# Optimization experiments

Hardware: AMD Instinct MI355X
Metric: run time of the kernel (lower is better)

## Reference

```python
import math
import jax, jax.numpy as jnp
import numpy as np

H, D_MODEL, D_K, D_V, SEQ, BATCH = 12, 768, 64, 64, 2048, 4


def setup_inputs() -> dict:
    key = jax.random.key(0)
    k1, k2, k3, k4, k5 = jax.random.split(key, 5)
    s = math.sqrt(0.02)
    return {
        "residual": jax.random.normal(k1, (BATCH, SEQ, D_MODEL), dtype=jnp.float32),
        "W_Q": jax.random.normal(k2, (H, D_MODEL, D_K), dtype=jnp.float32) * s,
        "W_K": jax.random.normal(k3, (H, D_MODEL, D_K), dtype=jnp.float32) * s,
        "W_V": jax.random.normal(k4, (H, D_MODEL, D_V), dtype=jnp.float32) * s,
        "W_O": jax.random.normal(k5, (H * D_V, D_MODEL), dtype=jnp.float32) * s,
    }


def reference(residual, W_Q, W_K, W_V, W_O):
    B, S, _ = residual.shape
    # Projections: h=head, m=d_model, k=d_k/d_v
    Q = jnp.einsum("hmk,bsm->hbsk", W_Q, residual)
    K = jnp.einsum("hmk,bsm->hbsk", W_K, residual)
    V = jnp.einsum("hmv,bsm->hbsv", W_V, residual)
    # Scores [h, b, s_q, s_k] + additive causal mask, scaled BEFORE softmax
    QK = jnp.einsum("hbqk,hbsk->hbqs", Q, K)
    causal = jnp.triu(jnp.ones((S, S), dtype=bool), k=1)
    mask = jnp.where(causal, -jnp.inf, 0.0).astype(QK.dtype)  # broadcasts over h,b
    soft = jax.nn.softmax((QK + mask) / math.sqrt(D_K), axis=-1)
    attn = jnp.einsum("hbqs,hbsv->hbqv", soft, V)
    # [h,b,q,v] -> [b,q,h*v]
    multi_head = jnp.transpose(attn, (1, 2, 0, 3)).reshape(B, S, -1)
    return jnp.einsum("nd,bqn->bqd", W_O, multi_head)
```

## Files before the change

kernel.cpp:

```cpp
#include <hip/hip_runtime.h>

typedef _Float16 f16;
typedef __fp16 h16x2 __attribute__((ext_vector_type(2)));
typedef _Float16 f16x8 __attribute__((ext_vector_type(8)));
typedef float f32x4 __attribute__((ext_vector_type(4)));

#define H_ 12
#define B_ 4
#define S_ 2048
#define DM 768
#define DK 64
#define HBSD ((size_t)H_ * B_ * S_ * DK)

__device__ __forceinline__ f16 f2h(float f) { return (f16)f; }

__device__ __forceinline__ void gl_lds16(const f16* g, f16* l) {
  __builtin_amdgcn_global_load_lds(
      (const __attribute__((address_space(1))) void*)g,
      (__attribute__((address_space(3))) void*)l, 16, 0, 0);
}


__global__ __launch_bounds__(256) void cast_x_kernel(const float* __restrict__ x,
                                                     f16* __restrict__ xb, int n4) {
  int i = blockIdx.x * 256 + threadIdx.x;
  if (i < n4) {
    float4 v = ((const float4*)x)[i];
    union { f16 h[4]; uint2 u; } pk;
    pk.h[0] = f2h(v.x); pk.h[1] = f2h(v.y); pk.h[2] = f2h(v.z); pk.h[3] = f2h(v.w);
    ((uint2*)xb)[i] = pk.u;
  }
}

__global__ __launch_bounds__(256) void tcast_qkv_kernel(const float* __restrict__ WQ,
                                                        const float* __restrict__ WK,
                                                        const float* __restrict__ WV,
                                                        f16* __restrict__ Wt) {
  __shared__ float L[64][65];
  const int m0 = blockIdx.x * 64, which = blockIdx.y, h = blockIdx.z;
  const float* in = (which == 0 ? WQ : which == 1 ? WK : WV) + (size_t)h * DM * DK;
  const int t = threadIdx.x;
  const int lr = t >> 2, lc = (t & 3) * 16;
  const float* ip = in + (size_t)(m0 + lr) * DK + lc;
#pragma unroll
  for (int i = 0; i < 4; i++) {
    float4 v = *(const float4*)(ip + i * 4);
    L[lr][lc + i * 4 + 0] = v.x;
    L[lr][lc + i * 4 + 1] = v.y;
    L[lr][lc + i * 4 + 2] = v.z;
    L[lr][lc + i * 4 + 3] = v.w;
  }
  __syncthreads();
  const int oc = t >> 2, om = (t & 3) * 16;
  union { f16 hh[16]; uint4 u[2]; } pk;
#pragma unroll
  for (int jx = 0; jx < 16; jx++) pk.hh[jx] = f2h(L[om + jx][oc]);
  f16* op = Wt + ((size_t)which * DM + h * DK + oc) * DM + m0 + om;
  *(uint4*)op = pk.u[0];
  *(uint4*)(op + 8) = pk.u[1];
}

__global__ __launch_bounds__(256) void tcast_wo_kernel(const float* __restrict__ WO,
                                                       f16* __restrict__ Wt) {
  __shared__ float L[64][65];
  const int n0 = blockIdx.x * 64, d0 = blockIdx.y * 64;
  const int t = threadIdx.x;
  const int lr = t >> 2, lc = (t & 3) * 16;
  const float* ip = WO + (size_t)(n0 + lr) * DM + d0 + lc;
#pragma unroll
  for (int i = 0; i < 4; i++) {
    float4 v = *(const float4*)(ip + i * 4);
    L[lr][lc + i * 4 + 0] = v.x;
    L[lr][lc + i * 4 + 1] = v.y;
    L[lr][lc + i * 4 + 2] = v.z;
    L[lr][lc + i * 4 + 3] = v.w;
  }
  __syncthreads();
  const int oc = t >> 2, om = (t & 3) * 16;
  union { f16 hh[16]; uint4 u[2]; } pk;
#pragma unroll
  for (int jx = 0; jx < 16; jx++) pk.hh[jx] = f2h(L[om + jx][oc]);
  f16* op = Wt + (size_t)(d0 + oc) * DM + n0 + om;
  *(uint4*)op = pk.u[0];
  *(uint4*)(op + 8) = pk.u[1];
}

template <int MODE>
__global__ __launch_bounds__(256) void gemm_bt_kernel(const f16* __restrict__ A,
                                                      const f16* __restrict__ Bt,
                                                      float* __restrict__ Cf,
                                                      f16* __restrict__ Cq,
                                                      f16* __restrict__ Vt, int N) {
  constexpr int K = 768;
  __shared__ __align__(16) f16 As[2 * 128 * 32];
  __shared__ __align__(16) f16 Bs[2 * 128 * 32];
  const int t = threadIdx.x;
  const int m0 = blockIdx.y * 128, n0 = blockIdx.x * 128;
  const int lane = t & 63, wave = t >> 6;
  const int l15 = lane & 15, quad = lane >> 4;
  const int qsw = quad ^ ((l15 >> 1) & 3);
  const int m_off = (wave & 1) * 64, n_off = (wave >> 1) * 64;
  const int r0 = t >> 2, ko = ((t & 3) ^ ((t >> 3) & 3)) * 8;
  const f16* Ag0 = A + (size_t)(m0 + r0) * K + ko;
  const f16* Ag1 = A + (size_t)(m0 + r0 + 64) * K + ko;
  const f16* Bg0 = Bt + (size_t)(n0 + r0) * K + ko;
  const f16* Bg1 = Bt + (size_t)(n0 + r0 + 64) * K + ko;

  f32x4 acc[4][4];
  const f32x4 z4 = {0.f, 0.f, 0.f, 0.f};
  for (int i = 0; i < 4; i++)
    for (int j = 0; j < 4; j++) acc[i][j] = z4;

  for (int kt = 0; kt < K; kt += 64) {
    __syncthreads();
#pragma unroll
    for (int s = 0; s < 2; s++) {
      gl_lds16(Ag0 + kt + s * 32, &As[s * 4096 + t * 8]);
      gl_lds16(Ag1 + kt + s * 32, &As[s * 4096 + 2048 + t * 8]);
      gl_lds16(Bg0 + kt + s * 32, &Bs[s * 4096 + t * 8]);
      gl_lds16(Bg1 + kt + s * 32, &Bs[s * 4096 + 2048 + t * 8]);
    }
    __syncthreads();
#pragma unroll
    for (int s = 0; s < 2; s++) {
      f16x8 af[4], bfr[4];
#pragma unroll
      for (int i = 0; i < 4; i++)
        af[i] = *(const f16x8*)&As[s * 4096 + (m_off + i * 16 + l15) * 32 + qsw * 8];
#pragma unroll
      for (int i = 0; i < 4; i++)
        bfr[i] = *(const f16x8*)&Bs[s * 4096 + (n_off + i * 16 + l15) * 32 + qsw * 8];
#pragma unroll
      for (int mi = 0; mi < 4; mi++)
#pragma unroll
        for (int ni = 0; ni < 4; ni++)
          acc[mi][ni] = __builtin_amdgcn_mfma_f32_16x16x32_f16(af[mi], bfr[ni],
                                                               acc[mi][ni], 0, 0, 0);
    }
  }

  if (MODE == 0) {
#pragma unroll
    for (int mi = 0; mi < 4; mi++) {
      int row = m0 + m_off + mi * 16 + quad * 4;
#pragma unroll
      for (int ni = 0; ni < 4; ni++) {
        int col = n0 + n_off + ni * 16 + l15;
#pragma unroll
        for (int r = 0; r < 4; r++) Cf[(size_t)(row + r) * N + col] = acc[mi][ni][r];
      }
    }
  } else {
#pragma unroll
    for (int mi = 0; mi < 4; mi++) {
      int srow = m0 + m_off + mi * 16 + quad * 4;
      int bb = srow >> 11, ss = srow & 2047;
#pragma unroll
      for (int ni = 0; ni < 4; ni++) {
        int n = n0 + n_off + ni * 16 + l15;
        int which = n / DM;
        int rr = n - which * DM;
        int h = rr >> 6, kk = rr & 63;
        if (which < 2) {
#pragma unroll
          for (int r = 0; r < 4; r++) {
            size_t dst = (size_t)which * HBSD +
                         ((size_t)((h * B_ + bb) * S_) + ss + r) * DK + kk;
            Cq[dst] = f2h(acc[mi][ni][r]);
          }
        } else {
          union { f16 hh[4]; uint2 u; } pk;
#pragma unroll
          for (int r = 0; r < 4; r++) pk.hh[r] = f2h(acc[mi][ni][r]);
          *(uint2*)&Vt[((size_t)(h * B_ + bb) * DK + kk) * S_ + ss] = pk.u;
        }
      }
    }
  }
}

__global__ __launch_bounds__(256, 3) void flash_kernel(const f16* __restrict__ Qg,
                                                       const f16* __restrict__ Kg,
                                                       const f16* __restrict__ Vtg,
                                                       f16* __restrict__ MH) {
  __shared__ __align__(16) f16 Ksh[2 * 64 * 32];
  __shared__ __align__(16) f16 Vsh[2 * 64 * 32];
  __shared__ __align__(16) f16 Ps[4][16 * 72];

  const int t = threadIdx.x, lane = t & 63, w = t >> 6;
  const int l15 = lane & 15, quad = lane >> 4;
  const int qsw = quad ^ ((l15 >> 1) & 3);
  const int bid = blockIdx.x;
  const int xcd = bid & 7, gi = bid >> 3;
  const int hbi = gi % 6, pr = gi / 6;
  const int hb = xcd * 6 + hbi;
  const int qbA = pr, qbB = 31 - pr;
  const int h = hb >> 2, b = hb & 3;
  const size_t base = (size_t)hb * S_ * DK;
  const f16* Qp = Qg + base;
  const f16* Kp = Kg + base;
  const f16* Vp = Vtg + base;
  const float c2 = 0.18033688011f;

  f16x8 aqA[2], aqB[2];
  {
    const f16* qa = Qp + (size_t)(qbA * 64 + w * 16 + l15) * DK + quad * 8;
    aqA[0] = *(const f16x8*)(qa);
    aqA[1] = *(const f16x8*)(qa + 32);
    const f16* qb_ = Qp + (size_t)(qbB * 64 + w * 16 + l15) * DK + quad * 8;
    aqB[0] = *(const f16x8*)(qb_);
    aqB[1] = *(const f16x8*)(qb_ + 32);
  }
  const int qlaneA = qbA * 64 + w * 16 + l15;
  const int qlaneB = qbB * 64 + w * 16 + l15;

  const int srow = t >> 2, scol = ((t & 3) ^ ((t >> 3) & 3)) * 8;
  const f16* Kst = Kp + (size_t)srow * DK + scol;
  const f16* Vst = Vp + (size_t)srow * S_ + scol;

  float mA = -1e30f, lA = 0.f, mB = -1e30f, lB = 0.f;
  f32x4 oA[4], oB[4];
  const f32x4 z4 = {0.f, 0.f, 0.f, 0.f};
#pragma unroll
  for (int ni = 0; ni < 4; ni++) { oA[ni] = z4; oB[ni] = z4; }

  auto do_job = [&](const f16x8* aq, float& m_s, float& l_s, f32x4* oacc,
                    int qlane, int kv0, bool diag) {
    f32x4 sa[4];
#pragma unroll
    for (int mi = 0; mi < 4; mi++) {
      f16x8 k0 = *(const f16x8*)&Ksh[(mi * 16 + l15) * 32 + qsw * 8];
      sa[mi] = __builtin_amdgcn_mfma_f32_16x16x32_f16(k0, aq[0], z4, 0, 0, 0);
    }
#pragma unroll
    for (int mi = 0; mi < 4; mi++) {
      f16x8 k1 = *(const f16x8*)&Ksh[2048 + (mi * 16 + l15) * 32 + qsw * 8];
      sa[mi] = __builtin_amdgcn_mfma_f32_16x16x32_f16(k1, aq[1], sa[mi], 0, 0, 0);
    }

    if (diag) {
#pragma unroll
      for (int mi = 0; mi < 4; mi++)
#pragma unroll
        for (int r = 0; r < 4; r++)
          if (kv0 + mi * 16 + quad * 4 + r > qlane) sa[mi][r] = -1e30f;
    }

    float mx = fmaxf(fmaxf(fmaxf(sa[0][0], sa[0][1]), fmaxf(sa[0][2], sa[0][3])),
                     fmaxf(fmaxf(sa[1][0], sa[1][1]), fmaxf(sa[1][2], sa[1][3])));
    float mx2 = fmaxf(fmaxf(fmaxf(sa[2][0], sa[2][1]), fmaxf(sa[2][2], sa[2][3])),
                      fmaxf(fmaxf(sa[3][0], sa[3][1]), fmaxf(sa[3][2], sa[3][3])));
    mx = fmaxf(mx, mx2);
    mx = fmaxf(mx, __shfl_xor(mx, 16));
    mx = fmaxf(mx, __shfl_xor(mx, 32));
    float pm = mx * c2;
    if (!__all(pm <= m_s + 8.f)) {
      float m2 = fmaxf(m_s, pm);
      float alpha = __builtin_exp2f(m_s - m2);
      l_s *= alpha;
#pragma unroll
      for (int ni = 0; ni < 4; ni++)
#pragma unroll
        for (int r = 0; r < 4; r++) oacc[ni][r] *= alpha;
      m_s = m2;
    }
    const float m2 = m_s;
    float rs = 0.f;
#pragma unroll
    for (int mi = 0; mi < 4; mi++)
#pragma unroll
      for (int r = 0; r < 4; r++) {
        float p = __builtin_exp2f(fmaf(sa[mi][r], c2, -m2));
        sa[mi][r] = p;
        rs += p;
      }
    rs += __shfl_xor(rs, 16);
    rs += __shfl_xor(rs, 32);
    l_s += rs;

#pragma unroll
    for (int mi = 0; mi < 4; mi++) {
      union { h16x2 h2[2]; uint2 u; } pk;
      pk.h2[0] = __builtin_amdgcn_cvt_pkrtz(sa[mi][0], sa[mi][1]);
      pk.h2[1] = __builtin_amdgcn_cvt_pkrtz(sa[mi][2], sa[mi][3]);
      *(uint2*)&Ps[w][l15 * 72 + mi * 16 + quad * 4] = pk.u;
    }

#pragma unroll
    for (int kc2 = 0; kc2 < 2; kc2++) {
      f16x8 ap = *(const f16x8*)&Ps[w][l15 * 72 + kc2 * 32 + quad * 8];
#pragma unroll
      for (int ni = 0; ni < 4; ni++) {
        f16x8 vf = *(const f16x8*)&Vsh[kc2 * 2048 + (ni * 16 + l15) * 32 + qsw * 8];
        oacc[ni] = __builtin_amdgcn_mfma_f32_16x16x32_f16(vf, ap, oacc[ni], 0, 0, 0);
      }
    }
  };

  for (int kt = 0; kt <= qbB; kt++) {
    const int kv0 = kt * 64;
    __syncthreads();
    gl_lds16(Kst + (size_t)kv0 * DK, &Ksh[t * 8]);
    gl_lds16(Kst + (size_t)kv0 * DK + 32, &Ksh[2048 + t * 8]);
    gl_lds16(Vst + kv0, &Vsh[t * 8]);
    gl_lds16(Vst + kv0 + 32, &Vsh[2048 + t * 8]);
    __syncthreads();

    do_job(aqB, mB, lB, oB, qlaneB, kv0, kt == qbB);
    if (kt <= qbA) do_job(aqA, mA, lA, oA, qlaneA, kv0, kt == qbA);
  }

  {
    float linv = 1.0f / lB;
    f16* dst = MH + ((size_t)b * S_ + qlaneB) * DM + h * DK + quad * 4;
#pragma unroll
    for (int ni = 0; ni < 4; ni++) {
      union { f16 hh[4]; uint2 u; } pk;
#pragma unroll
      for (int r = 0; r < 4; r++) pk.hh[r] = f2h(oB[ni][r] * linv);
      *(uint2*)(dst + ni * 16) = pk.u;
    }
  }
  {
    float linv = 1.0f / lA;
    f16* dst = MH + ((size_t)b * S_ + qlaneA) * DM + h * DK + quad * 4;
#pragma unroll
    for (int ni = 0; ni < 4; ni++) {
      union { f16 hh[4]; uint2 u; } pk;
#pragma unroll
      for (int r = 0; r < 4; r++) pk.hh[r] = f2h(oA[ni][r] * linv);
      *(uint2*)(dst + ni * 16) = pk.u;
    }
  }
}


extern "C" void kernel_launch(void* const* d_in, const int* in_sizes, int n_in,
                              void* d_out, int out_size, void* d_ws, size_t ws_size,
                              hipStream_t stream) {
  const float* residual = (const float*)d_in[0];
  const float* WQ = (const float*)d_in[1];
  const float* WK = (const float*)d_in[2];
  const float* WV = (const float*)d_in[3];
  const float* WO = (const float*)d_in[4];
  float* out = (float*)d_out;

  char* ws = (char*)d_ws;
  size_t off = 0;
  auto alloc = [&](size_t bytes) {
    void* p = ws + off;
    off += (bytes + 255) & ~(size_t)255;
    return p;
  };
  f16* xb = (f16*)alloc((size_t)B_ * S_ * DM * 2);
  f16* wqkv = (f16*)alloc((size_t)3 * DM * DM * 2);
  f16* wot = (f16*)alloc((size_t)DM * DM * 2);
  f16* qk = (f16*)alloc(2 * HBSD * 2);
  f16* vt = (f16*)alloc(HBSD * 2);
  f16* mh = (f16*)alloc((size_t)B_ * S_ * DM * 2);

  cast_x_kernel<<<(B_ * S_ * DM / 4 + 255) / 256, 256, 0, stream>>>(residual, xb,
                                                                    B_ * S_ * DM / 4);
  tcast_qkv_kernel<<<dim3(DM / 64, 3, H_), 256, 0, stream>>>(WQ, WK, WV, wqkv);
  tcast_wo_kernel<<<dim3(DM / 64, DM / 64), 256, 0, stream>>>(WO, wot);

  gemm_bt_kernel<1><<<dim3(3 * DM / 128, B_ * S_ / 128), 256, 0, stream>>>(
      xb, wqkv, nullptr, qk, vt, 3 * DM);

  flash_kernel<<<768, 256, 0, stream>>>(qk, qk + HBSD, vt, mh);

  gemm_bt_kernel<0><<<dim3(DM / 128, B_ * S_ / 128), 256, 0, stream>>>(
      mh, wot, out, nullptr, nullptr, DM);
}
```

Measured before the change: 217.3 us.

## Double-buffer K/V tiles in flash kernel with async prefetch and setprio

Splits the K and V shared-memory tiles into two buffers and issues the next tile's global-to-LDS loads before computing on the current one, waiting only on the older loads via a partial vmcnt. This aims to hide global load latency behind the MFMA work instead of stalling after each load. The MFMA sections are also wrapped in s_setprio, and the row-max is rewritten as a tree of three-input maxes. LDS use doubles for K/V, which may lower occupancy, and the hand-written waitcnt and barrier sequencing has to be exactly right to avoid races.

Result: slower. 228.0 us (+4.9%).

```diff
diff --git a/kernel.cpp b/kernel.cpp
--- a/kernel.cpp
+++ b/kernel.cpp
@@ -13,6 +13,9 @@
 #define HBSD ((size_t)H_ * B_ * S_ * DK)
 
 __device__ __forceinline__ f16 f2h(float f) { return (f16)f; }
+__device__ __forceinline__ float max3f(float a, float b, float c) {
+  return fmaxf(fmaxf(a, b), c);
+}
 
 __device__ __forceinline__ void gl_lds16(const f16* g, f16* l) {
   __builtin_amdgcn_global_load_lds(
@@ -183,8 +186,8 @@
                                                        const f16* __restrict__ Kg,
                                                        const f16* __restrict__ Vtg,
                                                        f16* __restrict__ MH) {
-  __shared__ __align__(16) f16 Ksh[2 * 64 * 32];
-  __shared__ __align__(16) f16 Vsh[2 * 64 * 32];
+  __shared__ __align__(16) f16 Ksh[2][4096];
+  __shared__ __align__(16) f16 Vsh[2][4096];
   __shared__ __align__(16) f16 Ps[4][16 * 72];
 
   const int t = threadIdx.x, lane = t & 63, w = t >> 6;
@@ -224,19 +227,28 @@
 #pragma unroll
   for (int ni = 0; ni < 4; ni++) { oA[ni] = z4; oB[ni] = z4; }
 
-  auto do_job = [&](const f16x8* aq, float& m_s, float& l_s, f32x4* oacc,
+  auto stage = [&](int buf, int kv0) {
+    gl_lds16(Kst + (size_t)kv0 * DK, &Ksh[buf][t * 8]);
+    gl_lds16(Kst + (size_t)kv0 * DK + 32, &Ksh[buf][2048 + t * 8]);
+    gl_lds16(Vst + kv0, &Vsh[buf][t * 8]);
+    gl_lds16(Vst + kv0 + 32, &Vsh[buf][2048 + t * 8]);
+  };
+
+  auto do_job = [&](int buf, const f16x8* aq, float& m_s, float& l_s, f32x4* oacc,
                     int qlane, int kv0, bool diag) {
     f32x4 sa[4];
-#pragma unroll
-    for (int mi = 0; mi < 4; mi++) {
-      f16x8 k0 = *(const f16x8*)&Ksh[(mi * 16 + l15) * 32 + qsw * 8];
+    __builtin_amdgcn_s_setprio(1);
+#pragma unroll
+    for (int mi = 0; mi < 4; mi++) {
+      f16x8 k0 = *(const f16x8*)&Ksh[buf][(mi * 16 + l15) * 32 + qsw * 8];
       sa[mi] = __builtin_amdgcn_mfma_f32_16x16x32_f16(k0, aq[0], z4, 0, 0, 0);
     }
 #pragma unroll
     for (int mi = 0; mi < 4; mi++) {
-      f16x8 k1 = *(const f16x8*)&Ksh[2048 + (mi * 16 + l15) * 32 + qsw * 8];
+      f16x8 k1 = *(const f16x8*)&Ksh[buf][2048 + (mi * 16 + l15) * 32 + qsw * 8];
       sa[mi] = __builtin_amdgcn_mfma_f32_16x16x32_f16(k1, aq[1], sa[mi], 0, 0, 0);
     }
+    __builtin_amdgcn_s_setprio(0);
 
     if (diag) {
 #pragma unroll
@@ -246,11 +258,12 @@
           if (kv0 + mi * 16 + quad * 4 + r > qlane) sa[mi][r] = -1e30f;
     }
 
-    float mx = fmaxf(fmaxf(fmaxf(sa[0][0], sa[0][1]), fmaxf(sa[0][2], sa[0][3])),
-                     fmaxf(fmaxf(sa[1][0], sa[1][1]), fmaxf(sa[1][2], sa[1][3])));
-    float mx2 = fmaxf(fmaxf(fmaxf(sa[2][0], sa[2][1]), fmaxf(sa[2][2], sa[2][3])),
-                      fmaxf(fmaxf(sa[3][0], sa[3][1]), fmaxf(sa[3][2], sa[3][3])));
-    mx = fmaxf(mx, mx2);
+    float g0 = max3f(sa[0][0], sa[0][1], sa[0][2]);
+    float g1 = max3f(sa[0][3], sa[1][0], sa[1][1]);
+    float g2 = max3f(sa[1][2], sa[1][3], sa[2][0]);
+    float g3 = max3f(sa[2][1], sa[2][2], sa[2][3]);
+    float g4 = max3f(sa[3][0], sa[3][1], sa[3][2]);
+    float mx = fmaxf(max3f(g0, g1, g2), max3f(g3, g4, sa[3][3]));
     mx = fmaxf(mx, __shfl_xor(mx, 16));
     mx = fmaxf(mx, __shfl_xor(mx, 32));
     float pm = mx * c2;
@@ -286,28 +299,35 @@
       *(uint2*)&Ps[w][l15 * 72 + mi * 16 + quad * 4] = pk.u;
     }
 
+    __builtin_amdgcn_s_setprio(1);
 #pragma unroll
     for (int kc2 = 0; kc2 < 2; kc2++) {
       f16x8 ap = *(const f16x8*)&Ps[w][l15 * 72 + kc2 * 32 + quad * 8];
 #pragma unroll
       for (int ni = 0; ni < 4; ni++) {
-        f16x8 vf = *(const f16x8*)&Vsh[kc2 * 2048 + (ni * 16 + l15) * 32 + qsw * 8];
+        f16x8 vf = *(const f16x8*)&Vsh[buf][kc2 * 2048 + (ni * 16 + l15) * 32 + qsw * 8];
         oacc[ni] = __builtin_amdgcn_mfma_f32_16x16x32_f16(vf, ap, oacc[ni], 0, 0, 0);
       }
     }
+    __builtin_amdgcn_s_setprio(0);
   };
 
+  stage(0, 0);
   for (int kt = 0; kt <= qbB; kt++) {
     const int kv0 = kt * 64;
-    __syncthreads();
-    gl_lds16(Kst + (size_t)kv0 * DK, &Ksh[t * 8]);
-    gl_lds16(Kst + (size_t)kv0 * DK + 32, &Ksh[2048 + t * 8]);
-    gl_lds16(Vst + kv0, &Vsh[t * 8]);
-    gl_lds16(Vst + kv0 + 32, &Vsh[2048 + t * 8]);
-    __syncthreads();
-
-    do_job(aqB, mB, lB, oB, qlaneB, kv0, kt == qbB);
-    if (kt <= qbA) do_job(aqA, mA, lA, oA, qlaneA, kv0, kt == qbA);
+    const int cur = kt & 1;
+    __builtin_amdgcn_s_barrier();
+    if (kt < qbB) {
+      stage(cur ^ 1, kv0 + 64);
+      asm volatile("s_waitcnt vmcnt(4)" ::: "memory");
+    } else {
+      asm volatile("s_waitcnt vmcnt(0)" ::: "memory");
+    }
+    __builtin_amdgcn_s_barrier();
+    __builtin_amdgcn_sched_barrier(0);
+
+    do_job(cur, aqB, mB, lB, oB, qlaneB, kv0, kt == qbB);
+    if (kt <= qbA) do_job(cur, aqA, mA, lA, oA, qlaneA, kv0, kt == qbA);
   }
 
   {
```
